# Kernel optimization log

Measured on AMD Instinct MI355X. Metric: run time of the kernel, lower is better.

## Reference

```python
import jax, jax.numpy as jnp
import numpy as np

D_MODEL = 2048
NUM_HEADS = 16
HEAD_DIM = D_MODEL // NUM_HEADS  # 128


def setup_inputs() -> dict:
    key = jax.random.key(0)
    ks = jax.random.split(key, 9)
    s = 0.02
    x = jax.random.normal(ks[0], (2, 2048, D_MODEL), dtype=jnp.float32)
    Wq = jax.random.normal(ks[1], (D_MODEL, D_MODEL), dtype=jnp.float32) * s
    bq = jnp.zeros((D_MODEL,), dtype=jnp.float32)
    Wk = jax.random.normal(ks[2], (D_MODEL, HEAD_DIM), dtype=jnp.float32) * s
    bk = jnp.zeros((HEAD_DIM,), dtype=jnp.float32)
    Wv = jax.random.normal(ks[3], (D_MODEL, HEAD_DIM), dtype=jnp.float32) * s
    bv = jnp.zeros((HEAD_DIM,), dtype=jnp.float32)
    Wo = jax.random.normal(ks[4], (D_MODEL, D_MODEL), dtype=jnp.float32) * s
    bo = jnp.zeros((D_MODEL,), dtype=jnp.float32)
    return {"x": x, "Wq": Wq, "bq": bq, "Wk": Wk, "bk": bk,
            "Wv": Wv, "bv": bv, "Wo": Wo, "bo": bo}


def reference(x, Wq, bq, Wk, bk, Wv, bv, Wo, bo):
    B, S, _ = x.shape
    # projections
    q = (x @ Wq + bq).reshape(B, S, NUM_HEADS, HEAD_DIM)  # [B,S,H,d]
    k = x @ Wk + bk  # [B,S,d] shared across heads (MQA)
    v = x @ Wv + bv  # [B,S,d]
    scale = 1.0 / jnp.sqrt(jnp.float32(HEAD_DIM))
    # QK^T with shared K: [B,H,Sq,Sk]
    scores = jnp.einsum('bqhd,bkd->bhqk', q, k) * scale
    attn = jax.nn.softmax(scores, axis=-1)
    # AV with shared V: [B,H,Sq,d]
    out = jnp.einsum('bhqk,bkd->bqhd', attn, v).reshape(B, S, D_MODEL)
    return out @ Wo + bo
```

## Files before the change

### kernel.cpp

```cpp
#include <hip/hip_runtime.h>


typedef __attribute__((ext_vector_type(8))) short short8;
typedef __attribute__((ext_vector_type(4))) float f32x4;
typedef __attribute__((ext_vector_type(4))) unsigned int uint4v;

__device__ __forceinline__ unsigned short f2bf(float f) {
  unsigned int u = __float_as_uint(f);
  u += 0x7FFF + ((u >> 16) & 1);
  return (unsigned short)(u >> 16);
}

__device__ __forceinline__ unsigned int pk2(float a, float b) {
  return (unsigned int)f2bf(a) | ((unsigned int)f2bf(b) << 16);
}

__device__ __forceinline__ void gll16(const void* g, void* lds) {
  __builtin_amdgcn_global_load_lds(
      (const __attribute__((address_space(1))) unsigned int*)g,
      (__attribute__((address_space(3))) unsigned int*)lds, 16, 0, 0);
}

__global__ __launch_bounds__(256)
void prep(const float* __restrict__ x, unsigned short* __restrict__ xb,
          const float* __restrict__ Wq, const float* __restrict__ Wo,
          const float* __restrict__ Wk, const float* __restrict__ Wv,
          unsigned short* __restrict__ wqkvt, unsigned short* __restrict__ wot) {
  __shared__ float tile[32][33];
  const int bid = blockIdx.x;
  const int t = threadIdx.x;

  if (bid < 4096) {
    int i = bid * 256 + t;
    const int stride = 4096 * 256;
    #pragma unroll
    for (int rep = 0; rep < 2; ++rep, i += stride) {
      float4 v = reinterpret_cast<const float4*>(x)[i];
      ushort4 o;
      o.x = f2bf(v.x); o.y = f2bf(v.y); o.z = f2bf(v.z); o.w = f2bf(v.w);
      reinterpret_cast<ushort4*>(xb)[i] = o;
    }
    return;
  }

  const float* W;
  unsigned short* Wt;
  int K = 2048, N, bx, by;
  if (bid < 12288) {
    int r = bid - 4096;
    int z = r >> 12, rr = r & 4095;
    bx = rr & 63; by = rr >> 6; N = 2048;
    W = z ? Wo : Wq;
    Wt = z ? wot : wqkvt;
  } else {
    int r = bid - 12288;
    int z = r >> 8, rr = r & 255;
    bx = rr & 3; by = rr >> 2; N = 128;
    W = z ? Wv : Wk;
    Wt = wqkvt + (size_t)(z ? 2176 : 2048) * 2048;
  }
  const int tx = t & 31, ty = t >> 5;
  const int n0 = bx * 32, k0 = by * 32;
  #pragma unroll
  for (int i = 0; i < 32; i += 8)
    tile[ty + i][tx] = W[(size_t)(k0 + ty + i) * N + n0 + tx];
  __syncthreads();
  #pragma unroll
  for (int i = 0; i < 32; i += 8)
    Wt[(size_t)(n0 + ty + i) * K + k0 + tx] = f2bf(tile[tx][ty + i]);
}

template <int MODE>
__global__ __launch_bounds__(256)
void gemm_nt(const unsigned short* __restrict__ A, const unsigned short* __restrict__ Bt,
             const float* __restrict__ b0, const float* __restrict__ b1,
             const float* __restrict__ b2,
             void* __restrict__ C, unsigned short* __restrict__ C2,
             unsigned short* __restrict__ C3, int M, int N, int K, float cmul) {
  __shared__ unsigned short lA[128 * 64];
  __shared__ unsigned short lB[64 * 64];
  const int t = threadIdx.x;
  const int lane = t & 63;
  const int w = t >> 6;
  const int wr = w >> 1, wc = w & 1;
  const int r15 = lane & 15, g4 = lane >> 4;
  const int tileM = blockIdx.y * 128;
  const int tileN = blockIdx.x * 64;

  f32x4 acc[4][2];
  #pragma unroll
  for (int i = 0; i < 4; i++)
    #pragma unroll
    for (int j = 0; j < 2; j++) acc[i][j] = (f32x4){0.f, 0.f, 0.f, 0.f};

  const int nkt = K >> 6;
  for (int kt = 0; kt < nkt; ++kt) {
    const int k0 = kt * 64;
    #pragma unroll
    for (int i = 0; i < 4; ++i) {
      int flat = i * 256 + t;
      int row = flat >> 3, gc = flat & 7;
      unsigned lb = (unsigned)(i * 256 + w * 64) * 16;
      gll16(A + (size_t)(tileM + row) * K + k0 + gc * 8, (char*)lA + lb);
    }
    #pragma unroll
    for (int i = 0; i < 2; ++i) {
      int flat = i * 256 + t;
      int row = flat >> 3, gc = flat & 7;
      unsigned lb = (unsigned)(i * 256 + w * 64) * 16;
      gll16(Bt + (size_t)(tileN + row) * K + k0 + gc * 8, (char*)lB + lb);
    }
    asm volatile("s_waitcnt vmcnt(0)" ::: "memory");
    __builtin_amdgcn_s_barrier();
    asm volatile("" ::: "memory");

    #pragma unroll
    for (int kk = 0; kk < 2; ++kk) {
      short8 af[4], bf[2];
      #pragma unroll
      for (int mt = 0; mt < 4; ++mt)
        af[mt] = *reinterpret_cast<const short8*>(&lA[(wr * 64 + mt * 16 + r15) * 64 + kk * 32 + g4 * 8]);
      #pragma unroll
      for (int nt = 0; nt < 2; ++nt)
        bf[nt] = *reinterpret_cast<const short8*>(&lB[(wc * 32 + nt * 16 + r15) * 64 + kk * 32 + g4 * 8]);
      #pragma unroll
      for (int mt = 0; mt < 4; ++mt)
        #pragma unroll
        for (int nt = 0; nt < 2; ++nt)
          acc[mt][nt] = __builtin_amdgcn_mfma_f32_16x16x32_bf16(af[mt], bf[nt], acc[mt][nt], 0, 0, 0);
    }
    asm volatile("" ::: "memory");
    __builtin_amdgcn_s_barrier();
  }

  #pragma unroll
  for (int mt = 0; mt < 4; ++mt) {
    #pragma unroll
    for (int nt = 0; nt < 2; ++nt) {
      int col = tileN + wc * 32 + nt * 16 + r15;
      #pragma unroll
      for (int r = 0; r < 4; ++r) {
        int row = tileM + wr * 64 + mt * 16 + g4 * 4 + r;
        float v = acc[mt][nt][r];
        if (MODE == 1) {
          ((float*)C)[(size_t)row * N + col] = v + b0[col];
        } else {
          if (col < 2048) {
            ((unsigned short*)C)[(size_t)row * 2048 + col] = f2bf((v + b0[col]) * cmul);
          } else if (col < 2176) {
            int dd = col - 2048;
            C2[(size_t)row * 128 + dd] = f2bf(v + b1[dd]);
          } else {
            int dd = col - 2176;
            int bb = row >> 11, s = row & 2047;
            C3[((size_t)bb * 128 + dd) * 2048 + s] = f2bf(v + b2[dd]);
          }
        }
      }
    }
  }
}

__global__ __launch_bounds__(256)
void flash_mqa(const unsigned short* __restrict__ qb, const unsigned short* __restrict__ kb,
               const unsigned short* __restrict__ vt, unsigned short* __restrict__ ob) {
  __shared__ unsigned short lK[2][64 * 128];
  __shared__ unsigned short lV[2][128 * 64];
  __shared__ unsigned short lP[4][16 * 64];

  const int t = threadIdx.x;
  const int lane = t & 63;
  const int w = t >> 6;
  const int r15 = lane & 15, g4 = lane >> 4;
  const int qt = blockIdx.x, hy = blockIdx.y, b = blockIdx.z;
  const int q0 = qt * 64 + w * 16;

  short8 qf[2][4];
  const size_t qrow = (size_t)(b * 2048 + q0 + r15);
  #pragma unroll
  for (int hh = 0; hh < 2; ++hh)
    #pragma unroll
    for (int kk = 0; kk < 4; ++kk)
      qf[hh][kk] = *reinterpret_cast<const short8*>(
          &qb[qrow * 2048 + (hy * 2 + hh) * 128 + kk * 32 + g4 * 8]);

  f32x4 oacc[2][8];
  #pragma unroll
  for (int hh = 0; hh < 2; ++hh)
    #pragma unroll
    for (int i = 0; i < 8; i++) oacc[hh][i] = (f32x4){0.f, 0.f, 0.f, 0.f};
  float m_q[2] = {-1e30f, -1e30f}, l_q[2] = {0.f, 0.f};

  const unsigned short* kbase = kb + (size_t)b * 2048 * 128;
  const unsigned short* vbase = vt + (size_t)b * 128 * 2048;

  auto stage = [&](int buf, int kv0) {
    #pragma unroll
    for (int i = 0; i < 4; ++i) {
      int flat = i * 256 + t;
      unsigned lb = (unsigned)(i * 256 + w * 64) * 16;
      { int row = flat >> 4, gc = flat & 15;
        gll16(kbase + (size_t)(kv0 + row) * 128 + ((gc ^ (row & 15)) << 3), (char*)lK[buf] + lb); }
      { int row = flat >> 3, gc = flat & 7;
        gll16(vbase + (size_t)row * 2048 + kv0 + ((gc ^ (row & 7)) << 3), (char*)lV[buf] + lb); }
    }
  };

  stage(0, 0);
  int cur = 0;
  for (int it = 0; it < 32; ++it) {
    if (it < 31) {
      stage(cur ^ 1, (it + 1) * 64);
      asm volatile("s_waitcnt vmcnt(8)" ::: "memory");
    } else {
      asm volatile("s_waitcnt vmcnt(0)" ::: "memory");
    }
    __builtin_amdgcn_s_barrier();
    asm volatile("" ::: "memory");

    const unsigned short* cK = lK[cur];
    const unsigned short* cV = lV[cur];

    #pragma unroll
    for (int hh = 0; hh < 2; ++hh) {
      f32x4 s[4];
      #pragma unroll
      for (int ct = 0; ct < 4; ct++) s[ct] = (f32x4){0.f, 0.f, 0.f, 0.f};
      #pragma unroll
      for (int kk = 0; kk < 4; ++kk) {
        #pragma unroll
        for (int ct = 0; ct < 4; ++ct) {
          const int krow = ct * 16 + r15;
          const int kg = (kk * 4 + g4) ^ (krow & 15);
          short8 kf = *reinterpret_cast<const short8*>(&cK[krow * 128 + kg * 8]);
          s[ct] = __builtin_amdgcn_mfma_f32_16x16x32_bf16(kf, qf[hh][kk], s[ct], 0, 0, 0);
        }
      }

      float mx = s[0][0];
      #pragma unroll
      for (int ct = 0; ct < 4; ++ct)
        #pragma unroll
        for (int r = 0; r < 4; ++r) mx = fmaxf(mx, s[ct][r]);
      mx = fmaxf(mx, __shfl_xor(mx, 16));
      mx = fmaxf(mx, __shfl_xor(mx, 32));
      if (__any(mx > m_q[hh] + 11.5416f)) {
        float mn = fmaxf(m_q[hh], mx);
        float rf = exp2f(m_q[hh] - mn);
        m_q[hh] = mn;
        l_q[hh] *= rf;
        #pragma unroll
        for (int ot = 0; ot < 8; ++ot)
          #pragma unroll
          for (int r = 0; r < 4; ++r) oacc[hh][ot][r] *= rf;
      }
      #pragma unroll
      for (int ct = 0; ct < 4; ++ct) {
        float p0 = exp2f(s[ct][0] - m_q[hh]);
        float p1 = exp2f(s[ct][1] - m_q[hh]);
        float p2 = exp2f(s[ct][2] - m_q[hh]);
        float p3 = exp2f(s[ct][3] - m_q[hh]);
        l_q[hh] += (p0 + p1) + (p2 + p3);
        const int gi = (ct * 4 + g4) ^ r15;
        *reinterpret_cast<uint2*>(&lP[w][r15 * 64 + gi * 4]) = make_uint2(pk2(p0, p1), pk2(p2, p3));
      }

      #pragma unroll
      for (int kk = 0; kk < 2; ++kk) {
        const int gA = (kk * 8 + g4 * 2) ^ r15;
        const int gB = (kk * 8 + g4 * 2 + 1) ^ r15;
        const uint2 wa = *reinterpret_cast<const uint2*>(&lP[w][r15 * 64 + gA * 4]);
        const uint2 wb = *reinterpret_cast<const uint2*>(&lP[w][r15 * 64 + gB * 4]);
        uint4v pw = {wa.x, wa.y, wb.x, wb.y};
        short8 pf = __builtin_bit_cast(short8, pw);
        #pragma unroll
        for (int ot = 0; ot < 8; ++ot) {
          const int vrow = ot * 16 + r15;
          const int vg = (kk * 4 + g4) ^ (vrow & 7);
          short8 vf = *reinterpret_cast<const short8*>(&cV[vrow * 64 + vg * 8]);
          oacc[hh][ot] = __builtin_amdgcn_mfma_f32_16x16x32_bf16(vf, pf, oacc[hh][ot], 0, 0, 0);
        }
      }
    }

    asm volatile("" ::: "memory");
    __builtin_amdgcn_s_barrier();
    cur ^= 1;
  }

  #pragma unroll
  for (int hh = 0; hh < 2; ++hh) {
    float l = l_q[hh];
    l += __shfl_xor(l, 16);
    l += __shfl_xor(l, 32);
    const float inv = 1.0f / l;
    const int row = q0 + r15;
    const size_t base = ((size_t)(b * 2048 + row)) * 2048 + (hy * 2 + hh) * 128;
    #pragma unroll
    for (int ot = 0; ot < 8; ++ot) {
      uint2 pw = make_uint2(pk2(oacc[hh][ot][0] * inv, oacc[hh][ot][1] * inv),
                            pk2(oacc[hh][ot][2] * inv, oacc[hh][ot][3] * inv));
      *reinterpret_cast<uint2*>(&ob[base + ot * 16 + g4 * 4]) = pw;
    }
  }
}

extern "C" void kernel_launch(void* const* d_in, const int* in_sizes, int n_in,
                              void* d_out, int out_size, void* d_ws, size_t ws_size,
                              hipStream_t stream) {
  const float* x  = (const float*)d_in[0];
  const float* Wq = (const float*)d_in[1];
  const float* bq = (const float*)d_in[2];
  const float* Wk = (const float*)d_in[3];
  const float* bk = (const float*)d_in[4];
  const float* Wv = (const float*)d_in[5];
  const float* bv = (const float*)d_in[6];
  const float* Wo = (const float*)d_in[7];
  const float* bo = (const float*)d_in[8];
  float* out = (float*)d_out;

  char* ws = (char*)d_ws;
  size_t off = 0;
  auto alloc = [&](size_t elems) {
    unsigned short* p = (unsigned short*)(ws + off);
    off += (elems * 2 + 255) & ~(size_t)255;
    return p;
  };
  unsigned short* xb    = alloc(8388608);
  unsigned short* qb    = alloc(8388608);
  unsigned short* ob    = alloc(8388608);
  unsigned short* wqkvt = alloc(4718592);
  unsigned short* wot   = alloc(4194304);
  unsigned short* kbuf  = alloc(524288);
  unsigned short* vtb   = alloc(524288);

  const float qscale = 0.08838834764831845f * 1.44269504088896f;

  prep<<<12800, 256, 0, stream>>>(x, xb, Wq, Wo, Wk, Wv, wqkvt, wot);

  gemm_nt<3><<<dim3(36, 32), 256, 0, stream>>>(xb, wqkvt, bq, bk, bv,
                                               qb, kbuf, vtb, 4096, 2304, 2048, qscale);
  flash_mqa<<<dim3(32, 8, 2), 256, 0, stream>>>(qb, kbuf, vtb, ob);
  gemm_nt<1><<<dim3(32, 32), 256, 0, stream>>>(ob, wot, bo, nullptr, nullptr,
                                               out, nullptr, nullptr, 4096, 2048, 2048, 1.0f);
}
```

Before: 258.4 us.

## Restructure flash MQA blocks to one head and 128 queries with 8 waves

Each flash-attention workgroup previously handled two heads for 64 query rows with 4 waves. It now handles one head for 128 query rows with 8 waves (512 threads). Each wave keeps a single head's accumulators, which cuts register pressure and should allow higher occupancy (launch bounds 512,4). The shared K/V tile is staged cooperatively by more threads, so each thread issues fewer loads and the wait count changes to match. The trade-off is that K/V staging is no longer shared across two heads per block. The same K/V data is now reused by 8 waves from the same head instead of 4 waves covering two heads.

```diff
diff --git a/kernel.cpp b/kernel.cpp
--- a/kernel.cpp
+++ b/kernel.cpp
@@ -161,44 +161,39 @@
   }
 }
 
-__global__ __launch_bounds__(256)
+__global__ __launch_bounds__(512, 4)
 void flash_mqa(const unsigned short* __restrict__ qb, const unsigned short* __restrict__ kb,
                const unsigned short* __restrict__ vt, unsigned short* __restrict__ ob) {
   __shared__ unsigned short lK[2][64 * 128];
   __shared__ unsigned short lV[2][128 * 64];
-  __shared__ unsigned short lP[4][16 * 64];
+  __shared__ unsigned short lP[8][16 * 64];
 
   const int t = threadIdx.x;
   const int lane = t & 63;
   const int w = t >> 6;
   const int r15 = lane & 15, g4 = lane >> 4;
-  const int qt = blockIdx.x, hy = blockIdx.y, b = blockIdx.z;
-  const int q0 = qt * 64 + w * 16;
-
-  short8 qf[2][4];
+  const int qt = blockIdx.x, h = blockIdx.y, b = blockIdx.z;
+  const int q0 = qt * 128 + w * 16;
+
+  short8 qf[4];
   const size_t qrow = (size_t)(b * 2048 + q0 + r15);
   #pragma unroll
-  for (int hh = 0; hh < 2; ++hh)
-    #pragma unroll
-    for (int kk = 0; kk < 4; ++kk)
-      qf[hh][kk] = *reinterpret_cast<const short8*>(
-          &qb[qrow * 2048 + (hy * 2 + hh) * 128 + kk * 32 + g4 * 8]);
-
-  f32x4 oacc[2][8];
-  #pragma unroll
-  for (int hh = 0; hh < 2; ++hh)
-    #pragma unroll
-    for (int i = 0; i < 8; i++) oacc[hh][i] = (f32x4){0.f, 0.f, 0.f, 0.f};
-  float m_q[2] = {-1e30f, -1e30f}, l_q[2] = {0.f, 0.f};
+  for (int kk = 0; kk < 4; ++kk)
+    qf[kk] = *reinterpret_cast<const short8*>(&qb[qrow * 2048 + h * 128 + kk * 32 + g4 * 8]);
+
+  f32x4 oacc[8];
+  #pragma unroll
+  for (int i = 0; i < 8; i++) oacc[i] = (f32x4){0.f, 0.f, 0.f, 0.f};
+  float m_q = -1e30f, l_q = 0.f;
 
   const unsigned short* kbase = kb + (size_t)b * 2048 * 128;
   const unsigned short* vbase = vt + (size_t)b * 128 * 2048;
 
   auto stage = [&](int buf, int kv0) {
     #pragma unroll
-    for (int i = 0; i < 4; ++i) {
-      int flat = i * 256 + t;
-      unsigned lb = (unsigned)(i * 256 + w * 64) * 16;
+    for (int i = 0; i < 2; ++i) {
+      int flat = i * 512 + t;
+      unsigned lb = (unsigned)(i * 512 + w * 64) * 16;
       { int row = flat >> 4, gc = flat & 15;
         gll16(kbase + (size_t)(kv0 + row) * 128 + ((gc ^ (row & 15)) << 3), (char*)lK[buf] + lb); }
       { int row = flat >> 3, gc = flat & 7;
@@ -211,7 +206,7 @@
   for (int it = 0; it < 32; ++it) {
     if (it < 31) {
       stage(cur ^ 1, (it + 1) * 64);
-      asm volatile("s_waitcnt vmcnt(8)" ::: "memory");
+      asm volatile("s_waitcnt vmcnt(4)" ::: "memory");
     } else {
       asm volatile("s_waitcnt vmcnt(0)" ::: "memory");
     }
@@ -221,65 +216,62 @@
     const unsigned short* cK = lK[cur];
     const unsigned short* cV = lV[cur];
 
-    #pragma unroll
-    for (int hh = 0; hh < 2; ++hh) {
-      f32x4 s[4];
-      #pragma unroll
-      for (int ct = 0; ct < 4; ct++) s[ct] = (f32x4){0.f, 0.f, 0.f, 0.f};
-      #pragma unroll
-      for (int kk = 0; kk < 4; ++kk) {
+    f32x4 s[4];
+    #pragma unroll
+    for (int ct = 0; ct < 4; ct++) s[ct] = (f32x4){0.f, 0.f, 0.f, 0.f};
+    #pragma unroll
+    for (int kk = 0; kk < 4; ++kk) {
+      #pragma unroll
+      for (int ct = 0; ct < 4; ++ct) {
+        const int krow = ct * 16 + r15;
+        const int kg = (kk * 4 + g4) ^ (krow & 15);
+        short8 kf = *reinterpret_cast<const short8*>(&cK[krow * 128 + kg * 8]);
+        s[ct] = __builtin_amdgcn_mfma_f32_16x16x32_bf16(kf, qf[kk], s[ct], 0, 0, 0);
+      }
+    }
+
+    float mx = s[0][0];
+    #pragma unroll
+    for (int ct = 0; ct < 4; ++ct)
+      #pragma unroll
+      for (int r = 0; r < 4; ++r) mx = fmaxf(mx, s[ct][r]);
+    mx = fmaxf(mx, __shfl_xor(mx, 16));
+    mx = fmaxf(mx, __shfl_xor(mx, 32));
+    if (__any(mx > m_q + 11.5416f)) {
+      float mn = fmaxf(m_q, mx);
+      float rf = exp2f(m_q - mn);
+      m_q = mn;
+      l_q *= rf;
+      #pragma unroll
+      for (int ot = 0; ot < 8; ++ot)
         #pragma unroll
-        for (int ct = 0; ct < 4; ++ct) {
-          const int krow = ct * 16 + r15;
-          const int kg = (kk * 4 + g4) ^ (krow & 15);
-          short8 kf = *reinterpret_cast<const short8*>(&cK[krow * 128 + kg * 8]);
-          s[ct] = __builtin_amdgcn_mfma_f32_16x16x32_bf16(kf, qf[hh][kk], s[ct], 0, 0, 0);
-        }
-      }
-
-      float mx = s[0][0];
-      #pragma unroll
-      for (int ct = 0; ct < 4; ++ct)
-        #pragma unroll
-        for (int r = 0; r < 4; ++r) mx = fmaxf(mx, s[ct][r]);
-      mx = fmaxf(mx, __shfl_xor(mx, 16));
-      mx = fmaxf(mx, __shfl_xor(mx, 32));
-      if (__any(mx > m_q[hh] + 11.5416f)) {
-        float mn = fmaxf(m_q[hh], mx);
-        float rf = exp2f(m_q[hh] - mn);
-        m_q[hh] = mn;
-        l_q[hh] *= rf;
-        #pragma unroll
-        for (int ot = 0; ot < 8; ++ot)
-          #pragma unroll
-          for (int r = 0; r < 4; ++r) oacc[hh][ot][r] *= rf;
-      }
-      #pragma unroll
-      for (int ct = 0; ct < 4; ++ct) {
-        float p0 = exp2f(s[ct][0] - m_q[hh]);
-        float p1 = exp2f(s[ct][1] - m_q[hh]);
-        float p2 = exp2f(s[ct][2] - m_q[hh]);
-        float p3 = exp2f(s[ct][3] - m_q[hh]);
-        l_q[hh] += (p0 + p1) + (p2 + p3);
-        const int gi = (ct * 4 + g4) ^ r15;
-        *reinterpret_cast<uint2*>(&lP[w][r15 * 64 + gi * 4]) = make_uint2(pk2(p0, p1), pk2(p2, p3));
-      }
-
-      #pragma unroll
-      for (int kk = 0; kk < 2; ++kk) {
-        const int gA = (kk * 8 + g4 * 2) ^ r15;
-        const int gB = (kk * 8 + g4 * 2 + 1) ^ r15;
-        const uint2 wa = *reinterpret_cast<const uint2*>(&lP[w][r15 * 64 + gA * 4]);
-        const uint2 wb = *reinterpret_cast<const uint2*>(&lP[w][r15 * 64 + gB * 4]);
-        uint4v pw = {wa.x, wa.y, wb.x, wb.y};
-        short8 pf = __builtin_bit_cast(short8, pw);
-        #pragma unroll
-        for (int ot = 0; ot < 8; ++ot) {
-          const int vrow = ot * 16 + r15;
-          const int vg = (kk * 4 + g4) ^ (vrow & 7);
-          short8 vf = *reinterpret_cast<const short8*>(&cV[vrow * 64 + vg * 8]);
-          oacc[hh][ot] = __builtin_amdgcn_mfma_f32_16x16x32_bf16(vf, pf, oacc[hh][ot], 0, 0, 0);
-        }
+        for (int r = 0; r < 4; ++r) oacc[ot][r] *= rf;
+    }
+    #pragma unroll
+    for (int ct = 0; ct < 4; ++ct) {
+      float p0 = exp2f(s[ct][0] - m_q);
+      float p1 = exp2f(s[ct][1] - m_q);
+      float p2 = exp2f(s[ct][2] - m_q);
+      float p3 = exp2f(s[ct][3] - m_q);
+      l_q += (p0 + p1) + (p2 + p3);
+      const int gi = (ct * 4 + g4) ^ r15;
+      *reinterpret_cast<uint2*>(&lP[w][r15 * 64 + gi * 4]) = make_uint2(pk2(p0, p1), pk2(p2, p3));
+    }
+
+    #pragma unroll
+    for (int kk = 0; kk < 2; ++kk) {
+      const int gA = (kk * 8 + g4 * 2) ^ r15;
+      const int gB = (kk * 8 + g4 * 2 + 1) ^ r15;
+      const uint2 wa = *reinterpret_cast<const uint2*>(&lP[w][r15 * 64 + gA * 4]);
+      const uint2 wb = *reinterpret_cast<const uint2*>(&lP[w][r15 * 64 + gB * 4]);
+      uint4v pw = {wa.x, wa.y, wb.x, wb.y};
+      short8 pf = __builtin_bit_cast(short8, pw);
+      #pragma unroll
+      for (int ot = 0; ot < 8; ++ot) {
+        const int vrow = ot * 16 + r15;
+        const int vg = (kk * 4 + g4) ^ (vrow & 7);
+        short8 vf = *reinterpret_cast<const short8*>(&cV[vrow * 64 + vg * 8]);
+        oacc[ot] = __builtin_amdgcn_mfma_f32_16x16x32_bf16(vf, pf, oacc[ot], 0, 0, 0);
       }
     }
 
@@ -288,20 +280,17 @@
     cur ^= 1;
   }
 
-  #pragma unroll
-  for (int hh = 0; hh < 2; ++hh) {
-    float l = l_q[hh];
-    l += __shfl_xor(l, 16);
-    l += __shfl_xor(l, 32);
-    const float inv = 1.0f / l;
-    const int row = q0 + r15;
-    const size_t base = ((size_t)(b * 2048 + row)) * 2048 + (hy * 2 + hh) * 128;
-    #pragma unroll
-    for (int ot = 0; ot < 8; ++ot) {
-      uint2 pw = make_uint2(pk2(oacc[hh][ot][0] * inv, oacc[hh][ot][1] * inv),
-                            pk2(oacc[hh][ot][2] * inv, oacc[hh][ot][3] * inv));
-      *reinterpret_cast<uint2*>(&ob[base + ot * 16 + g4 * 4]) = pw;
-    }
+  float l = l_q;
+  l += __shfl_xor(l, 16);
+  l += __shfl_xor(l, 32);
+  const float inv = 1.0f / l;
+  const int row = q0 + r15;
+  const size_t base = ((size_t)(b * 2048 + row)) * 2048 + h * 128;
+  #pragma unroll
+  for (int ot = 0; ot < 8; ++ot) {
+    uint2 pw = make_uint2(pk2(oacc[ot][0] * inv, oacc[ot][1] * inv),
+                          pk2(oacc[ot][2] * inv, oacc[ot][3] * inv));
+    *reinterpret_cast<uint2*>(&ob[base + ot * 16 + g4 * 4]) = pw;
   }
 }
 
@@ -340,7 +329,7 @@
 
   gemm_nt<3><<<dim3(36, 32), 256, 0, stream>>>(xb, wqkvt, bq, bk, bv,
                                                qb, kbuf, vtb, 4096, 2304, 2048, qscale);
-  flash_mqa<<<dim3(32, 8, 2), 256, 0, stream>>>(qb, kbuf, vtb, ob);
+  flash_mqa<<<dim3(16, 16, 2), 512, 0, stream>>>(qb, kbuf, vtb, ob);
   gemm_nt<1><<<dim3(32, 32), 256, 0, stream>>>(ob, wot, bo, nullptr, nullptr,
                                                out, nullptr, nullptr, 4096, 2048, 2048, 1.0f);
 }
```

Measured after the change: 246.1 us. 1.05x faster.
